# Kernel optimization log

Hardware: AMD Instinct MI355X
Metric: run time of the kernel (lower is better)

## Reference

```python
import jax, jax.numpy as jnp
import numpy as np

HID, OUT = 128, 64
N_SOTU, N_TAXON = 500_000, 200_000
E_TT, E_TS, E_LBL = 200_000, 1_000_000, 500_000


def _sage(x_src, x_dst, src, dst, wl, bl, wr):
    """PyG SAGEConv (mean aggr): lin_l(mean of neighbor msgs) + lin_r(x_dst)."""
    n_dst = x_dst.shape[0]
    agg = jax.ops.segment_sum(x_src[src], dst, num_segments=n_dst)
    deg = jax.ops.segment_sum(jnp.ones(src.shape[0], x_src.dtype), dst, num_segments=n_dst)
    agg = agg / jnp.maximum(deg, 1.0)[:, None]
    return agg @ wl + bl + x_dst @ wr


def setup_inputs() -> dict:
    key = jax.random.key(0)
    ks = iter(jax.random.split(key, 40))

    def w(shape):
        fan_in = shape[0]
        return (jax.random.normal(next(ks), shape, jnp.float32) / np.sqrt(fan_in)).astype(jnp.float32)

    def ri(n, hi):
        return jax.random.randint(next(ks), (n,), 0, hi, dtype=jnp.int32)

    inp = {
        "sotu_ids": jnp.arange(N_SOTU, dtype=jnp.int32),
        "taxon_ids": jnp.arange(N_TAXON, dtype=jnp.int32),
        "ett_src": ri(E_TT, N_TAXON),
        "ett_dst": ri(E_TT, N_TAXON),
        "ets_src": ri(E_TS, N_TAXON),
        "ets_dst": ri(E_TS, N_SOTU),
        "elbl_row": ri(E_LBL, N_SOTU),
        "elbl_col": ri(E_LBL, N_TAXON),
        # embeddings
        "sotu_emb": jax.random.normal(next(ks), (N_SOTU, HID), jnp.float32),
        "taxon_emb": jax.random.normal(next(ks), (N_TAXON, HID), jnp.float32),
        # SOTU encoder: conv1 (taxon->taxon), conv2/3 (taxon->sotu), lin
        "s1_wl": w((HID, HID)), "s1_bl": jnp.zeros((HID,), jnp.float32), "s1_wr": w((HID, HID)),
        "s2_wl": w((HID, HID)), "s2_bl": jnp.zeros((HID,), jnp.float32), "s2_wr": w((HID, HID)),
        "s3_wl": w((HID, HID)), "s3_bl": jnp.zeros((HID,), jnp.float32), "s3_wr": w((HID, HID)),
        "sl_w": w((HID, OUT)), "sl_b": jnp.zeros((OUT,), jnp.float32),
        # Taxon encoder: conv1, conv2, lin
        "t1_wl": w((HID, HID)), "t1_bl": jnp.zeros((HID,), jnp.float32), "t1_wr": w((HID, HID)),
        "t2_wl": w((HID, HID)), "t2_bl": jnp.zeros((HID,), jnp.float32), "t2_wr": w((HID, HID)),
        "tl_w": w((HID, OUT)), "tl_b": jnp.zeros((OUT,), jnp.float32),
        # Edge decoder MLP
        "d1_w": w((2 * OUT, OUT)), "d1_b": jnp.zeros((OUT,), jnp.float32),
        "d2_w": w((OUT, 1)), "d2_b": jnp.zeros((1,), jnp.float32),
    }
    return inp


def reference(sotu_ids, taxon_ids, ett_src, ett_dst, ets_src, ets_dst,
              elbl_row, elbl_col, sotu_emb, taxon_emb,
              s1_wl, s1_bl, s1_wr, s2_wl, s2_bl, s2_wr, s3_wl, s3_bl, s3_wr,
              sl_w, sl_b, t1_wl, t1_bl, t1_wr, t2_wl, t2_bl, t2_wr, tl_w, tl_b,
              d1_w, d1_b, d2_w, d2_b):
    # embedding lookup
    x_sotu = sotu_emb[sotu_ids]          # [N_SOTU, HID]
    x_taxon = taxon_emb[taxon_ids]       # [N_TAXON, HID]
    # SOTU encoder
    taxon_x = jax.nn.relu(_sage(x_taxon, x_taxon, ett_src, ett_dst, s1_wl, s1_bl, s1_wr))
    sotu_x = jax.nn.relu(_sage(x_taxon, x_sotu, ets_src, ets_dst, s2_wl, s2_bl, s2_wr))
    sotu_x = jax.nn.relu(_sage(taxon_x, sotu_x, ets_src, ets_dst, s3_wl, s3_bl, s3_wr))
    z_sotu = sotu_x @ sl_w + sl_b        # [N_SOTU, OUT]
    # Taxon encoder
    tx = jax.nn.relu(_sage(x_taxon, x_taxon, ett_src, ett_dst, t1_wl, t1_bl, t1_wr))
    tx = jax.nn.relu(_sage(tx, tx, ett_src, ett_dst, t2_wl, t2_bl, t2_wr))
    z_taxon = tx @ tl_w + tl_b           # [N_TAXON, OUT]
    # Edge decoder: gather endpoints, fused MLP
    z = jnp.concatenate([z_sotu[elbl_row], z_taxon[elbl_col]], axis=-1)  # [E_LBL, 2*OUT]
    h = jax.nn.relu(z @ d1_w + d1_b)
    return (h @ d2_w + d2_b).reshape(-1)  # [E_LBL]
```

## Files before the change

### kernel.cpp

```cpp
#include <hip/hip_runtime.h>

#define HID 128
#define OUTD 64
#define N_SOTU 500000
#define N_TAXON 200000
#define E_TT 200000
#define E_TS 1000000
#define E_LBL 500000
#define HALF_S 250000
#define SCAN_TILE 2048

typedef short s16x8 __attribute__((ext_vector_type(8)));
typedef float f32x4 __attribute__((ext_vector_type(4)));

__device__ __forceinline__ unsigned short f2bf(float f) {
    unsigned u = __builtin_bit_cast(unsigned, f);
    u += 0x7FFFu + ((u >> 16) & 1u);
    return (unsigned short)(u >> 16);
}
__device__ __forceinline__ float bf2f(unsigned short h) {
    unsigned u = ((unsigned)h) << 16;
    return __builtin_bit_cast(float, u);
}

__global__ void hist_kernel(const int* __restrict__ dst, int n, int* __restrict__ rp) {
    int e = blockIdx.x * 256 + threadIdx.x;
    if (e < n) atomicAdd(&rp[dst[e]], 1);
}

__global__ __launch_bounds__(256) void scan1_kernel(int* __restrict__ a, int n, int* __restrict__ bsums) {
    __shared__ int tsum[256];
    const int t = threadIdx.x;
    const int base = blockIdx.x * SCAN_TILE + t * 8;
    int v[8]; int s = 0;
#pragma unroll
    for (int i = 0; i < 8; i++) {
        int x = (base + i < n) ? a[base + i] : 0;
        s += x; v[i] = s;
    }
    tsum[t] = s;
    __syncthreads();
    for (int off = 1; off < 256; off <<= 1) {
        int x = (t >= off) ? tsum[t - off] : 0;
        __syncthreads();
        tsum[t] += x;
        __syncthreads();
    }
    const int prev = (t > 0) ? tsum[t - 1] : 0;
#pragma unroll
    for (int i = 0; i < 8; i++)
        if (base + i < n) a[base + i] = v[i] + prev;
    if (t == 255) bsums[blockIdx.x] = tsum[255];
}

__global__ __launch_bounds__(256) void scan2_kernel(int* __restrict__ bsums, int nb) {
    __shared__ int tsum[256];
    const int t = threadIdx.x;
    tsum[t] = (t < nb) ? bsums[t] : 0;
    __syncthreads();
    for (int off = 1; off < 256; off <<= 1) {
        int x = (t >= off) ? tsum[t - off] : 0;
        __syncthreads();
        tsum[t] += x;
        __syncthreads();
    }
    if (t < nb) bsums[t] = tsum[t];
}

__global__ __launch_bounds__(256) void scan3_kernel(int* __restrict__ a, int n, const int* __restrict__ bsums) {
    const int b = blockIdx.x;
    if (b == 0) return;
    const int add = bsums[b - 1];
    const int base = b * SCAN_TILE + threadIdx.x * 8;
#pragma unroll
    for (int i = 0; i < 8; i++)
        if (base + i < n) a[base + i] += add;
}

__global__ void fill_kernel(const int* __restrict__ src, const int* __restrict__ dst, int n,
                            int* __restrict__ rp, int* __restrict__ sl) {
    int e = blockIdx.x * 256 + threadIdx.x;
    if (e < n) {
        int pos = atomicSub(&rp[dst[e]], 1) - 1;
        sl[pos] = src[e];
    }
}

__global__ __launch_bounds__(256) void gather_kernel(
    const float* __restrict__ xf, const unsigned short* __restrict__ xb,
    const int* __restrict__ xids,
    const int* __restrict__ rp, const int* __restrict__ sl,
    int n_dst_total, int n_edges, int lo, int rows,
    unsigned short* __restrict__ agg)
{
    const int g = blockIdx.x * 16 + (threadIdx.x >> 4);
    if (g >= rows) return;
    const int d = lo + g;
    const int l = threadIdx.x & 15;
    const int start = rp[d];
    const int end = (d + 1 < n_dst_total) ? rp[d + 1] : n_edges;
    float acc[8] = {0.f, 0.f, 0.f, 0.f, 0.f, 0.f, 0.f, 0.f};
    for (int j = start; j < end; ++j) {
        int s = sl[j];
        if (xids) s = xids[s];
        if (xf) {
            const float* p = xf + (size_t)s * HID + l * 8;
            float4 v0 = *(const float4*)p;
            float4 v1 = *(const float4*)(p + 4);
            acc[0] += v0.x; acc[1] += v0.y; acc[2] += v0.z; acc[3] += v0.w;
            acc[4] += v1.x; acc[5] += v1.y; acc[6] += v1.z; acc[7] += v1.w;
        } else {
            s16x8 b = *(const s16x8*)(xb + (size_t)s * HID + l * 8);
#pragma unroll
            for (int i = 0; i < 8; i++) acc[i] += bf2f((unsigned short)b[i]);
        }
    }
    const float inv = (end > start) ? 1.0f / (float)(end - start) : 0.0f;
    s16x8 o;
#pragma unroll
    for (int i = 0; i < 8; i++) o[i] = (short)f2bf(acc[i] * inv);
    *(s16x8*)(agg + (size_t)g * HID + l * 8) = o;
}

__device__ __forceinline__ int wt_idx(int n, int k) {
    return n * 256 + ((((k >> 3) ^ n) & 31) << 3) + (k & 7);
}

__global__ __launch_bounds__(256) void sage_kernel(
    int n_rows, int row0,
    const unsigned short* __restrict__ agg,
    const float* __restrict__ xf, const unsigned short* __restrict__ xb,
    const int* __restrict__ xids,
    const float* __restrict__ wl, const float* __restrict__ wr,
    const float* __restrict__ bl,
    unsigned short* __restrict__ out)
{
    __shared__ __align__(16) unsigned short WT[128 * 256];
    for (int idx = threadIdx.x; idx < 128 * 128; idx += 256) {
        int n = idx & 127, k = idx >> 7;
        WT[wt_idx(n, k)]       = f2bf(wl[idx]);
        WT[wt_idx(n, k + 128)] = f2bf(wr[idx]);
    }
    __syncthreads();
    const int lane = threadIdx.x & 63, wid = threadIdx.x >> 6;
    const int l16 = lane & 15, q = lane >> 4;
    const int n_tiles = n_rows >> 4;
    const int stride = gridDim.x * 4;
    for (int tile = blockIdx.x * 4 + wid; tile < n_tiles; tile += stride) {
        const int base = tile << 4;
        const int lrow = base + l16;
        const size_t xrow = xids ? (size_t)xids[lrow] : (size_t)(row0 + lrow);
        f32x4 acc[8] = {};
#pragma unroll
        for (int ks = 0; ks < 4; ks++) {
            s16x8 a = *(const s16x8*)(agg + (size_t)lrow * HID + ks * 32 + q * 8);
            const int kb = ks * 32 + q * 8;
#pragma unroll
            for (int nt = 0; nt < 8; nt++) {
                s16x8 b = *(const s16x8*)&WT[wt_idx(nt * 16 + l16, kb)];
                acc[nt] = __builtin_amdgcn_mfma_f32_16x16x32_bf16(a, b, acc[nt], 0, 0, 0);
            }
        }
#pragma unroll
        for (int ks = 0; ks < 4; ks++) {
            s16x8 a;
            if (xf) {
                const float* xp = xf + xrow * HID + ks * 32 + q * 8;
                float4 v0 = *(const float4*)xp;
                float4 v1 = *(const float4*)(xp + 4);
                a[0] = (short)f2bf(v0.x); a[1] = (short)f2bf(v0.y);
                a[2] = (short)f2bf(v0.z); a[3] = (short)f2bf(v0.w);
                a[4] = (short)f2bf(v1.x); a[5] = (short)f2bf(v1.y);
                a[6] = (short)f2bf(v1.z); a[7] = (short)f2bf(v1.w);
            } else {
                a = *(const s16x8*)(xb + xrow * HID + ks * 32 + q * 8);
            }
            const int kb = 128 + ks * 32 + q * 8;
#pragma unroll
            for (int nt = 0; nt < 8; nt++) {
                s16x8 b = *(const s16x8*)&WT[wt_idx(nt * 16 + l16, kb)];
                acc[nt] = __builtin_amdgcn_mfma_f32_16x16x32_bf16(a, b, acc[nt], 0, 0, 0);
            }
        }
#pragma unroll
        for (int nt = 0; nt < 8; nt++) {
            const int n = nt * 16 + l16;
            const float bv = bl[n];
#pragma unroll
            for (int i = 0; i < 4; i++) {
                float v = acc[nt][i] + bv;
                out[(size_t)(base + q * 4 + i) * HID + n] = f2bf(fmaxf(v, 0.0f));
            }
        }
    }
}

__global__ __launch_bounds__(256) void proj_kernel(
    int n_nodes, const unsigned short* __restrict__ x,
    const float* __restrict__ w, const float* __restrict__ bias, unsigned short* __restrict__ z)
{
    const int lane = threadIdx.x & 63, wid = threadIdx.x >> 6;
    const int l16 = lane & 15, q = lane >> 4;
    s16x8 bfr[4][4];
#pragma unroll
    for (int ks = 0; ks < 4; ks++)
#pragma unroll
        for (int nt = 0; nt < 4; nt++)
#pragma unroll
            for (int i = 0; i < 8; i++)
                bfr[ks][nt][i] = (short)f2bf(w[(ks * 32 + q * 8 + i) * OUTD + nt * 16 + l16]);
    const int n_tiles = n_nodes >> 4;
    const int stride = gridDim.x * 4;
    for (int tile = blockIdx.x * 4 + wid; tile < n_tiles; tile += stride) {
        const int base = tile << 4;
        const size_t mrow = (size_t)(base + l16);
        f32x4 acc[4] = {};
#pragma unroll
        for (int ks = 0; ks < 4; ks++) {
            s16x8 a = *(const s16x8*)(x + mrow * HID + ks * 32 + q * 8);
#pragma unroll
            for (int nt = 0; nt < 4; nt++)
                acc[nt] = __builtin_amdgcn_mfma_f32_16x16x32_bf16(a, bfr[ks][nt], acc[nt], 0, 0, 0);
        }
#pragma unroll
        for (int nt = 0; nt < 4; nt++) {
            const int n = nt * 16 + l16;
            const float bv = bias[n];
#pragma unroll
            for (int i = 0; i < 4; i++)
                z[(size_t)(base + q * 4 + i) * OUTD + n] = f2bf(acc[nt][i] + bv);
        }
    }
}

__global__ __launch_bounds__(256) void dec_kernel(
    const int* __restrict__ erow, const int* __restrict__ ecol,
    const unsigned short* __restrict__ zs, const unsigned short* __restrict__ zt,
    const float* __restrict__ w1, const float* __restrict__ b1,
    const float* __restrict__ w2, const float* __restrict__ b2,
    float* __restrict__ out)
{
    const int lane = threadIdx.x & 63, wid = threadIdx.x >> 6;
    const int l16 = lane & 15, q = lane >> 4;
    s16x8 bfr[4][4];
#pragma unroll
    for (int ks = 0; ks < 4; ks++)
#pragma unroll
        for (int nt = 0; nt < 4; nt++)
#pragma unroll
            for (int i = 0; i < 8; i++)
                bfr[ks][nt][i] = (short)f2bf(w1[(ks * 32 + q * 8 + i) * OUTD + nt * 16 + l16]);
    float b1v[4], w2v[4];
#pragma unroll
    for (int nt = 0; nt < 4; nt++) {
        b1v[nt] = b1[nt * 16 + l16];
        w2v[nt] = w2[nt * 16 + l16];
    }
    const float b2v = b2[0];
    const int n_tiles = E_LBL >> 4;
    for (int tile = blockIdx.x * 4 + wid; tile < n_tiles; tile += gridDim.x * 4) {
        const int em = tile * 16 + l16;
        const size_t r = (size_t)erow[em], c = (size_t)ecol[em];
        f32x4 acc[4] = {};
        s16x8 a0 = *(const s16x8*)(zs + r * OUTD + q * 8);
        s16x8 a1 = *(const s16x8*)(zs + r * OUTD + 32 + q * 8);
        s16x8 a2 = *(const s16x8*)(zt + c * OUTD + q * 8);
        s16x8 a3 = *(const s16x8*)(zt + c * OUTD + 32 + q * 8);
#pragma unroll
        for (int nt = 0; nt < 4; nt++) {
            acc[nt] = __builtin_amdgcn_mfma_f32_16x16x32_bf16(a0, bfr[0][nt], acc[nt], 0, 0, 0);
            acc[nt] = __builtin_amdgcn_mfma_f32_16x16x32_bf16(a1, bfr[1][nt], acc[nt], 0, 0, 0);
            acc[nt] = __builtin_amdgcn_mfma_f32_16x16x32_bf16(a2, bfr[2][nt], acc[nt], 0, 0, 0);
            acc[nt] = __builtin_amdgcn_mfma_f32_16x16x32_bf16(a3, bfr[3][nt], acc[nt], 0, 0, 0);
        }
        float s[4] = {0.0f, 0.0f, 0.0f, 0.0f};
#pragma unroll
        for (int nt = 0; nt < 4; nt++)
#pragma unroll
            for (int i = 0; i < 4; i++)
                s[i] += fmaxf(acc[nt][i] + b1v[nt], 0.0f) * w2v[nt];
#pragma unroll
        for (int off = 8; off >= 1; off >>= 1)
#pragma unroll
            for (int i = 0; i < 4; i++)
                s[i] += __shfl_down(s[i], off, 16);
        if (l16 == 0) {
#pragma unroll
            for (int i = 0; i < 4; i++)
                out[tile * 16 + q * 4 + i] = s[i] + b2v;
        }
    }
}

static void build_csr(const int* src, const int* dst, int n_edges, int n_dst,
                      int* rp, int* sl, int* bsums, hipStream_t stream) {
    hipMemsetAsync(rp, 0, (size_t)n_dst * 4, stream);
    hist_kernel<<<(n_edges + 255) / 256, 256, 0, stream>>>(dst, n_edges, rp);
    const int nb = (n_dst + SCAN_TILE - 1) / SCAN_TILE;
    scan1_kernel<<<nb, 256, 0, stream>>>(rp, n_dst, bsums);
    scan2_kernel<<<1, 256, 0, stream>>>(bsums, nb);
    scan3_kernel<<<nb, 256, 0, stream>>>(rp, n_dst, bsums);
    fill_kernel<<<(n_edges + 255) / 256, 256, 0, stream>>>(src, dst, n_edges, rp, sl);
}

extern "C" void kernel_launch(void* const* d_in, const int* in_sizes, int n_in,
                              void* d_out, int out_size, void* d_ws, size_t ws_size,
                              hipStream_t stream) {
    (void)in_sizes; (void)n_in; (void)out_size; (void)ws_size;
    const int* sotu_ids  = (const int*)d_in[0];
    const int* taxon_ids = (const int*)d_in[1];
    const int* ett_src   = (const int*)d_in[2];
    const int* ett_dst   = (const int*)d_in[3];
    const int* ets_src   = (const int*)d_in[4];
    const int* ets_dst   = (const int*)d_in[5];
    const int* elbl_row  = (const int*)d_in[6];
    const int* elbl_col  = (const int*)d_in[7];
    const float* sotu_emb  = (const float*)d_in[8];
    const float* taxon_emb = (const float*)d_in[9];
    const float* s1_wl = (const float*)d_in[10]; const float* s1_bl = (const float*)d_in[11]; const float* s1_wr = (const float*)d_in[12];
    const float* s2_wl = (const float*)d_in[13]; const float* s2_bl = (const float*)d_in[14]; const float* s2_wr = (const float*)d_in[15];
    const float* s3_wl = (const float*)d_in[16]; const float* s3_bl = (const float*)d_in[17]; const float* s3_wr = (const float*)d_in[18];
    const float* sl_w  = (const float*)d_in[19]; const float* sl_b  = (const float*)d_in[20];
    const float* t1_wl = (const float*)d_in[21]; const float* t1_bl = (const float*)d_in[22]; const float* t1_wr = (const float*)d_in[23];
    const float* t2_wl = (const float*)d_in[24]; const float* t2_bl = (const float*)d_in[25]; const float* t2_wr = (const float*)d_in[26];
    const float* tl_w  = (const float*)d_in[27]; const float* tl_b  = (const float*)d_in[28];
    const float* d1_w  = (const float*)d_in[29]; const float* d1_b  = (const float*)d_in[30];
    const float* d2_w  = (const float*)d_in[31]; const float* d2_b  = (const float*)d_in[32];
    float* out = (float*)d_out;

    char* ws = (char*)d_ws;
    size_t off = 0;
    auto alloc = [&](size_t bytes) { void* p = ws + off; off = (off + bytes + 255) & ~(size_t)255; return p; };
    unsigned short* agg     = (unsigned short*)alloc((size_t)HALF_S * HID * 2);
    unsigned short* taxon_x = (unsigned short*)alloc((size_t)N_TAXON * HID * 2);
    unsigned short* tx1     = (unsigned short*)alloc((size_t)N_TAXON * HID * 2);
    unsigned short* sotu_x  = (unsigned short*)alloc((size_t)N_SOTU * HID * 2);
    unsigned short* z_taxon = (unsigned short*)alloc((size_t)N_TAXON * OUTD * 2);
    int* rp_ts = (int*)alloc((size_t)N_SOTU * 4);
    int* sl_ts = (int*)alloc((size_t)E_TS * 4);
    int* rp_tt = (int*)alloc((size_t)N_TAXON * 4);
    int* sl_tt = (int*)alloc((size_t)E_TT * 4);
    int* bsums = (int*)alloc(256 * 4);
    unsigned short* z_sotu = agg;

    build_csr(ett_src, ett_dst, E_TT, N_TAXON, rp_tt, sl_tt, bsums, stream);
    build_csr(ets_src, ets_dst, E_TS, N_SOTU, rp_ts, sl_ts, bsums, stream);

    gather_kernel<<<(N_TAXON + 15) / 16, 256, 0, stream>>>(
        taxon_emb, nullptr, taxon_ids, rp_tt, sl_tt, N_TAXON, E_TT, 0, N_TAXON, agg);
    sage_kernel<<<512, 256, 0, stream>>>(N_TAXON, 0, agg, taxon_emb, nullptr, taxon_ids,
                                         s1_wl, s1_wr, s1_bl, taxon_x);
    sage_kernel<<<512, 256, 0, stream>>>(N_TAXON, 0, agg, taxon_emb, nullptr, taxon_ids,
                                         t1_wl, t1_wr, t1_bl, tx1);

    gather_kernel<<<(N_TAXON + 15) / 16, 256, 0, stream>>>(
        nullptr, tx1, nullptr, rp_tt, sl_tt, N_TAXON, E_TT, 0, N_TAXON, agg);
    sage_kernel<<<512, 256, 0, stream>>>(N_TAXON, 0, agg, nullptr, tx1, nullptr,
                                         t2_wl, t2_wr, t2_bl, tx1);
    proj_kernel<<<1024, 256, 0, stream>>>(N_TAXON, tx1, tl_w, tl_b, z_taxon);

    for (int h = 0; h < 2; ++h) {
        int lo = h * HALF_S;
        gather_kernel<<<(HALF_S + 15) / 16, 256, 0, stream>>>(
            taxon_emb, nullptr, taxon_ids, rp_ts, sl_ts, N_SOTU, E_TS, lo, HALF_S, agg);
        sage_kernel<<<512, 256, 0, stream>>>(HALF_S, lo, agg, sotu_emb, nullptr, sotu_ids + lo,
                                             s2_wl, s2_wr, s2_bl, sotu_x + (size_t)lo * HID);
    }
    for (int h = 0; h < 2; ++h) {
        int lo = h * HALF_S;
        gather_kernel<<<(HALF_S + 15) / 16, 256, 0, stream>>>(
            nullptr, taxon_x, nullptr, rp_ts, sl_ts, N_SOTU, E_TS, lo, HALF_S, agg);
        sage_kernel<<<512, 256, 0, stream>>>(HALF_S, lo, agg, nullptr, sotu_x, nullptr,
                                             s3_wl, s3_wr, s3_bl, sotu_x + (size_t)lo * HID);
    }
    proj_kernel<<<1024, 256, 0, stream>>>(N_SOTU, sotu_x, sl_w, sl_b, z_sotu);

    dec_kernel<<<1024, 256, 0, stream>>>(elbl_row, elbl_col, z_sotu, z_taxon,
                                         d1_w, d1_b, d2_w, d2_b, out);
}
```

Baseline: 1.625 ms.

## Fuse neighbor gather-mean into SAGE MFMA kernel and pre-convert embeddings to bf16

Removes the separate gather kernel and the aggregation buffer it wrote. Each SAGE tile now walks its CSR neighbor list itself, accumulates the mean in registers and feeds it directly to the MFMA. The fp32 embeddings are first converted to bf16 once, so gathers read half the bytes and the ids indirection is gone. In exchange, the s1/t1 layers now each redo the same taxon gather, each lane holds a 32-float accumulator, and neighbor loads are serialized per row inside the MFMA wave, which may raise latency and register pressure.

```diff
diff --git a/kernel.cpp b/kernel.cpp
--- a/kernel.cpp
+++ b/kernel.cpp
@@ -7,7 +7,6 @@
 #define E_TT 200000
 #define E_TS 1000000
 #define E_LBL 500000
-#define HALF_S 250000
 #define SCAN_TILE 2048
 
 typedef short s16x8 __attribute__((ext_vector_type(8)));
@@ -21,6 +20,22 @@
 __device__ __forceinline__ float bf2f(unsigned short h) {
     unsigned u = ((unsigned)h) << 16;
     return __builtin_bit_cast(float, u);
+}
+
+__global__ __launch_bounds__(256) void conv_kernel(const float* __restrict__ emb,
+                                                   const int* __restrict__ ids, int n_rows,
+                                                   unsigned short* __restrict__ outb) {
+    int t = blockIdx.x * 256 + threadIdx.x;
+    int row = t >> 4;
+    if (row >= n_rows) return;
+    int part = t & 15;
+    const float* p = emb + (size_t)ids[row] * HID + part * 8;
+    float4 v0 = *(const float4*)p;
+    float4 v1 = *(const float4*)(p + 4);
+    s16x8 o;
+    o[0] = (short)f2bf(v0.x); o[1] = (short)f2bf(v0.y); o[2] = (short)f2bf(v0.z); o[3] = (short)f2bf(v0.w);
+    o[4] = (short)f2bf(v1.x); o[5] = (short)f2bf(v1.y); o[6] = (short)f2bf(v1.z); o[7] = (short)f2bf(v1.w);
+    *(s16x8*)(outb + (size_t)row * HID + part * 8) = o;
 }
 
 __global__ void hist_kernel(const int* __restrict__ dst, int n, int* __restrict__ rp) {
@@ -86,51 +101,15 @@
     }
 }
 
-__global__ __launch_bounds__(256) void gather_kernel(
-    const float* __restrict__ xf, const unsigned short* __restrict__ xb,
-    const int* __restrict__ xids,
-    const int* __restrict__ rp, const int* __restrict__ sl,
-    int n_dst_total, int n_edges, int lo, int rows,
-    unsigned short* __restrict__ agg)
-{
-    const int g = blockIdx.x * 16 + (threadIdx.x >> 4);
-    if (g >= rows) return;
-    const int d = lo + g;
-    const int l = threadIdx.x & 15;
-    const int start = rp[d];
-    const int end = (d + 1 < n_dst_total) ? rp[d + 1] : n_edges;
-    float acc[8] = {0.f, 0.f, 0.f, 0.f, 0.f, 0.f, 0.f, 0.f};
-    for (int j = start; j < end; ++j) {
-        int s = sl[j];
-        if (xids) s = xids[s];
-        if (xf) {
-            const float* p = xf + (size_t)s * HID + l * 8;
-            float4 v0 = *(const float4*)p;
-            float4 v1 = *(const float4*)(p + 4);
-            acc[0] += v0.x; acc[1] += v0.y; acc[2] += v0.z; acc[3] += v0.w;
-            acc[4] += v1.x; acc[5] += v1.y; acc[6] += v1.z; acc[7] += v1.w;
-        } else {
-            s16x8 b = *(const s16x8*)(xb + (size_t)s * HID + l * 8);
-#pragma unroll
-            for (int i = 0; i < 8; i++) acc[i] += bf2f((unsigned short)b[i]);
-        }
-    }
-    const float inv = (end > start) ? 1.0f / (float)(end - start) : 0.0f;
-    s16x8 o;
-#pragma unroll
-    for (int i = 0; i < 8; i++) o[i] = (short)f2bf(acc[i] * inv);
-    *(s16x8*)(agg + (size_t)g * HID + l * 8) = o;
-}
-
 __device__ __forceinline__ int wt_idx(int n, int k) {
     return n * 256 + ((((k >> 3) ^ n) & 31) << 3) + (k & 7);
 }
 
-__global__ __launch_bounds__(256) void sage_kernel(
-    int n_rows, int row0,
-    const unsigned short* __restrict__ agg,
-    const float* __restrict__ xf, const unsigned short* __restrict__ xb,
-    const int* __restrict__ xids,
+__global__ __launch_bounds__(256) void fsage_kernel(
+    int n_rows,
+    const int* __restrict__ rp, const int* __restrict__ sl, int n_edges,
+    const unsigned short* __restrict__ xa,
+    const unsigned short* __restrict__ xd,
     const float* __restrict__ wl, const float* __restrict__ wr,
     const float* __restrict__ bl,
     unsigned short* __restrict__ out)
@@ -148,12 +127,28 @@
     const int stride = gridDim.x * 4;
     for (int tile = blockIdx.x * 4 + wid; tile < n_tiles; tile += stride) {
         const int base = tile << 4;
-        const int lrow = base + l16;
-        const size_t xrow = xids ? (size_t)xids[lrow] : (size_t)(row0 + lrow);
+        const int row = base + l16;
+        const int start = rp[row];
+        const int end = (row + 1 < n_rows) ? rp[row + 1] : n_edges;
+        float ga[32];
+#pragma unroll
+        for (int i = 0; i < 32; i++) ga[i] = 0.0f;
+        for (int j = start; j < end; ++j) {
+            const size_t s = (size_t)sl[j];
+#pragma unroll
+            for (int ks = 0; ks < 4; ks++) {
+                s16x8 v = *(const s16x8*)(xa + s * HID + ks * 32 + q * 8);
+#pragma unroll
+                for (int i = 0; i < 8; i++) ga[ks * 8 + i] += bf2f((unsigned short)v[i]);
+            }
+        }
+        const float inv = (end > start) ? 1.0f / (float)(end - start) : 0.0f;
         f32x4 acc[8] = {};
 #pragma unroll
         for (int ks = 0; ks < 4; ks++) {
-            s16x8 a = *(const s16x8*)(agg + (size_t)lrow * HID + ks * 32 + q * 8);
+            s16x8 a;
+#pragma unroll
+            for (int i = 0; i < 8; i++) a[i] = (short)f2bf(ga[ks * 8 + i] * inv);
             const int kb = ks * 32 + q * 8;
 #pragma unroll
             for (int nt = 0; nt < 8; nt++) {
@@ -163,18 +158,7 @@
         }
 #pragma unroll
         for (int ks = 0; ks < 4; ks++) {
-            s16x8 a;
-            if (xf) {
-                const float* xp = xf + xrow * HID + ks * 32 + q * 8;
-                float4 v0 = *(const float4*)xp;
-                float4 v1 = *(const float4*)(xp + 4);
-                a[0] = (short)f2bf(v0.x); a[1] = (short)f2bf(v0.y);
-                a[2] = (short)f2bf(v0.z); a[3] = (short)f2bf(v0.w);
-                a[4] = (short)f2bf(v1.x); a[5] = (short)f2bf(v1.y);
-                a[6] = (short)f2bf(v1.z); a[7] = (short)f2bf(v1.w);
-            } else {
-                a = *(const s16x8*)(xb + xrow * HID + ks * 32 + q * 8);
-            }
+            s16x8 a = *(const s16x8*)(xd + (size_t)row * HID + ks * 32 + q * 8);
             const int kb = 128 + ks * 32 + q * 8;
 #pragma unroll
             for (int nt = 0; nt < 8; nt++) {
@@ -331,49 +315,40 @@
     char* ws = (char*)d_ws;
     size_t off = 0;
     auto alloc = [&](size_t bytes) { void* p = ws + off; off = (off + bytes + 255) & ~(size_t)255; return p; };
-    unsigned short* agg     = (unsigned short*)alloc((size_t)HALF_S * HID * 2);
-    unsigned short* taxon_x = (unsigned short*)alloc((size_t)N_TAXON * HID * 2);
-    unsigned short* tx1     = (unsigned short*)alloc((size_t)N_TAXON * HID * 2);
-    unsigned short* sotu_x  = (unsigned short*)alloc((size_t)N_SOTU * HID * 2);
-    unsigned short* z_taxon = (unsigned short*)alloc((size_t)N_TAXON * OUTD * 2);
+    unsigned short* xb_taxon = (unsigned short*)alloc((size_t)N_TAXON * HID * 2);
+    unsigned short* xb_sotu  = (unsigned short*)alloc((size_t)N_SOTU * HID * 2);
+    unsigned short* taxon_x  = (unsigned short*)alloc((size_t)N_TAXON * HID * 2);
+    unsigned short* tx1      = (unsigned short*)alloc((size_t)N_TAXON * HID * 2);
+    unsigned short* tx2      = (unsigned short*)alloc((size_t)N_TAXON * HID * 2);
+    unsigned short* sotu_x   = (unsigned short*)alloc((size_t)N_SOTU * HID * 2);
+    unsigned short* sotu_x2  = (unsigned short*)alloc((size_t)N_SOTU * HID * 2);
+    unsigned short* z_taxon  = (unsigned short*)alloc((size_t)N_TAXON * OUTD * 2);
+    unsigned short* z_sotu   = (unsigned short*)alloc((size_t)N_SOTU * OUTD * 2);
     int* rp_ts = (int*)alloc((size_t)N_SOTU * 4);
     int* sl_ts = (int*)alloc((size_t)E_TS * 4);
     int* rp_tt = (int*)alloc((size_t)N_TAXON * 4);
     int* sl_tt = (int*)alloc((size_t)E_TT * 4);
     int* bsums = (int*)alloc(256 * 4);
-    unsigned short* z_sotu = agg;
+
+    conv_kernel<<<(N_TAXON * 16 + 255) / 256, 256, 0, stream>>>(taxon_emb, taxon_ids, N_TAXON, xb_taxon);
+    conv_kernel<<<(N_SOTU * 16 + 255) / 256, 256, 0, stream>>>(sotu_emb, sotu_ids, N_SOTU, xb_sotu);
 
     build_csr(ett_src, ett_dst, E_TT, N_TAXON, rp_tt, sl_tt, bsums, stream);
     build_csr(ets_src, ets_dst, E_TS, N_SOTU, rp_ts, sl_ts, bsums, stream);
 
-    gather_kernel<<<(N_TAXON + 15) / 16, 256, 0, stream>>>(
-        taxon_emb, nullptr, taxon_ids, rp_tt, sl_tt, N_TAXON, E_TT, 0, N_TAXON, agg);
-    sage_kernel<<<512, 256, 0, stream>>>(N_TAXON, 0, agg, taxon_emb, nullptr, taxon_ids,
-                                         s1_wl, s1_wr, s1_bl, taxon_x);
-    sage_kernel<<<512, 256, 0, stream>>>(N_TAXON, 0, agg, taxon_emb, nullptr, taxon_ids,
-                                         t1_wl, t1_wr, t1_bl, tx1);
-
-    gather_kernel<<<(N_TAXON + 15) / 16, 256, 0, stream>>>(
-        nullptr, tx1, nullptr, rp_tt, sl_tt, N_TAXON, E_TT, 0, N_TAXON, agg);
-    sage_kernel<<<512, 256, 0, stream>>>(N_TAXON, 0, agg, nullptr, tx1, nullptr,
-                                         t2_wl, t2_wr, t2_bl, tx1);
-    proj_kernel<<<1024, 256, 0, stream>>>(N_TAXON, tx1, tl_w, tl_b, z_taxon);
-
-    for (int h = 0; h < 2; ++h) {
-        int lo = h * HALF_S;
-        gather_kernel<<<(HALF_S + 15) / 16, 256, 0, stream>>>(
-            taxon_emb, nullptr, taxon_ids, rp_ts, sl_ts, N_SOTU, E_TS, lo, HALF_S, agg);
-        sage_kernel<<<512, 256, 0, stream>>>(HALF_S, lo, agg, sotu_emb, nullptr, sotu_ids + lo,
-                                             s2_wl, s2_wr, s2_bl, sotu_x + (size_t)lo * HID);
-    }
-    for (int h = 0; h < 2; ++h) {
-        int lo = h * HALF_S;
-        gather_kernel<<<(HALF_S + 15) / 16, 256, 0, stream>>>(
-            nullptr, taxon_x, nullptr, rp_ts, sl_ts, N_SOTU, E_TS, lo, HALF_S, agg);
-        sage_kernel<<<512, 256, 0, stream>>>(HALF_S, lo, agg, nullptr, sotu_x, nullptr,
-                                             s3_wl, s3_wr, s3_bl, sotu_x + (size_t)lo * HID);
-    }
-    proj_kernel<<<1024, 256, 0, stream>>>(N_SOTU, sotu_x, sl_w, sl_b, z_sotu);
+    fsage_kernel<<<512, 256, 0, stream>>>(N_TAXON, rp_tt, sl_tt, E_TT, xb_taxon, xb_taxon,
+                                          s1_wl, s1_wr, s1_bl, taxon_x);
+    fsage_kernel<<<512, 256, 0, stream>>>(N_TAXON, rp_tt, sl_tt, E_TT, xb_taxon, xb_taxon,
+                                          t1_wl, t1_wr, t1_bl, tx1);
+    fsage_kernel<<<512, 256, 0, stream>>>(N_TAXON, rp_tt, sl_tt, E_TT, tx1, tx1,
+                                          t2_wl, t2_wr, t2_bl, tx2);
+    proj_kernel<<<1024, 256, 0, stream>>>(N_TAXON, tx2, tl_w, tl_b, z_taxon);
+
+    fsage_kernel<<<512, 256, 0, stream>>>(N_SOTU, rp_ts, sl_ts, E_TS, xb_taxon, xb_sotu,
+                                          s2_wl, s2_wr, s2_bl, sotu_x);
+    fsage_kernel<<<512, 256, 0, stream>>>(N_SOTU, rp_ts, sl_ts, E_TS, taxon_x, sotu_x,
+                                          s3_wl, s3_wr, s3_bl, sotu_x2);
+    proj_kernel<<<1024, 256, 0, stream>>>(N_SOTU, sotu_x2, sl_w, sl_b, z_sotu);
 
     dec_kernel<<<1024, 256, 0, stream>>>(elbl_row, elbl_col, z_sotu, z_taxon,
                                          d1_w, d1_b, d2_w, d2_b, out);
```

Measured after the change: 1.825 ms. 1.12x slower.
